# Optimization experiments

Measured on AMD Instinct MI355X. Metric: run time of the kernel, lower is better.

The kernel has to match this reference:

```python
import jax, jax.numpy as jnp
import numpy as np

NUM_BINS = 50


def _power_spectrum(x):
    # fft2 over last two dims, |.|^2, fftshift — matches torch.fft.fft2/fftshift
    freq = jnp.fft.fft2(x, axes=(-2, -1))
    power = jnp.abs(freq) ** 2
    return jnp.fft.fftshift(power, axes=(-2, -1))


def _radial_bin_ids(H, W, num_bins):
    # Static precompute of the bin index for every pixel (replaces the
    # triple-nested mask loop with a single segment reduction).
    cy, cx = H // 2, W // 2
    y = jnp.arange(H, dtype=jnp.float32) - cy
    x = jnp.arange(W, dtype=jnp.float32) - cx
    radius = jnp.sqrt(y[:, None] ** 2 + x[None, :] ** 2)  # [H, W]
    max_radius = min(H, W) // 2
    bin_edges = jnp.linspace(0.0, float(max_radius), num_bins + 1)
    # bin i covers [edges[i], edges[i+1]); radius >= max_radius -> overflow bin
    ids = jnp.clip(jnp.searchsorted(bin_edges, radius.ravel(), side='right') - 1, 0, num_bins)
    return ids  # [H*W], values in [0, num_bins] (num_bins = dropped overflow)


def _radial_profile(power, num_bins=NUM_BINS):
    B, C, H, W = power.shape
    ids = _radial_bin_ids(H, W, num_bins)
    pflat = power.reshape(B, C, H * W)
    seg_sum = jax.vmap(jax.vmap(lambda p: jax.ops.segment_sum(p, ids, num_segments=num_bins + 1)))(pflat)
    counts = jax.ops.segment_sum(jnp.ones((H * W,), power.dtype), ids, num_segments=num_bins + 1)
    profile = jnp.where(counts > 0, seg_sum / jnp.maximum(counts, 1.0), 0.0)
    return profile[..., :num_bins]  # [B, C, num_bins]


def setup_inputs() -> dict:
    key = jax.random.key(0)
    k1, k2 = jax.random.split(key)
    x = jax.random.normal(k1, (16, 3, 512, 512), dtype=jnp.float32)
    reference = jax.random.normal(k2, (16, 3, 512, 512), dtype=jnp.float32)
    return {"x": x, "reference": reference}


def reference(x, reference):
    power_x = _power_spectrum(x)
    profile_x = _radial_profile(power_x)
    power_ref = _power_spectrum(reference)
    profile_ref = _radial_profile(power_ref)
    B = profile_x.shape[0]
    logits_x = profile_x.reshape(B, -1)
    logits_ref = profile_ref.reshape(B, -1)
    # F.kl_div(log_p, q).sum(1) == sum q * (log q - log p)
    log_p = jax.nn.log_softmax(logits_x, axis=1)
    log_q = jax.nn.log_softmax(logits_ref, axis=1)
    q = jnp.exp(log_q)
    divergence = jnp.sum(q * (log_q - log_p), axis=1)  # [B]
    return divergence
```

## Files before the change

### kernel.cpp

```cpp
#include <hip/hip_runtime.h>


#define NIMG 96
#define NB 50
#define NCOL 257
#define PHYS(k) ((k) ^ (((k) >> 3) & 7))

typedef unsigned int uint32;
typedef unsigned short ushort16;

__device__ __forceinline__ float2 cadd(float2 a, float2 b){ return make_float2(a.x+b.x, a.y+b.y); }
__device__ __forceinline__ float2 csub(float2 a, float2 b){ return make_float2(a.x-b.x, a.y-b.y); }
__device__ __forceinline__ float2 cmul(float2 a, float2 b){
  return make_float2(fmaf(a.x, b.x, -(a.y*b.y)), fmaf(a.x, b.y, a.y*b.x));
}
__device__ __forceinline__ float2 mul_mi(float2 a){ return make_float2(a.y, -a.x); }

__device__ __forceinline__ uint32 bfpack(float re, float im) {
  uint32 ur = __float_as_uint(re); ur += 0x7FFFu + ((ur >> 16) & 1u);
  uint32 ui = __float_as_uint(im); ui += 0x7FFFu + ((ui >> 16) & 1u);
  return (ur & 0xFFFF0000u) | (ui >> 16);
}
__device__ __forceinline__ float2 bfunpack(uint32 u) {
  return make_float2(__uint_as_float(u & 0xFFFF0000u), __uint_as_float(u << 16));
}

struct C8 { float2 m0, m1, m2, m3, m4, m5, m6, m7; };

__device__ __forceinline__ C8 fft8(C8 v) {
  const float C = 0.70710678118654752f;
  float2 t0=cadd(v.m0,v.m4), t1=csub(v.m0,v.m4);
  float2 t2=cadd(v.m2,v.m6), t3m=mul_mi(csub(v.m2,v.m6));
  float2 E0=cadd(t0,t2), E1=cadd(t1,t3m), E2=csub(t0,t2), E3=csub(t1,t3m);
  float2 s0=cadd(v.m1,v.m5), s1=csub(v.m1,v.m5);
  float2 s2=cadd(v.m3,v.m7), s3m=mul_mi(csub(v.m3,v.m7));
  float2 O0=cadd(s0,s2), O1=cadd(s1,s3m), O2=csub(s0,s2), O3=csub(s1,s3m);
  O1 = make_float2(C*(O1.x+O1.y), C*(O1.y-O1.x));
  O2 = mul_mi(O2);
  O3 = make_float2(C*(O3.y-O3.x), -C*(O3.x+O3.y));
  C8 r;
  r.m0=cadd(E0,O0); r.m4=csub(E0,O0);
  r.m1=cadd(E1,O1); r.m5=csub(E1,O1);
  r.m2=cadd(E2,O2); r.m6=csub(E2,O2);
  r.m3=cadd(E3,O3); r.m7=csub(E3,O3);
  return r;
}

#define TWAP1(X, W) do { float2 t_ = (W);                               \
  X.m1=cmul(X.m1,t_); t_=cmul(t_,(W));                                  \
  X.m2=cmul(X.m2,t_); t_=cmul(t_,(W));                                  \
  X.m3=cmul(X.m3,t_); t_=cmul(t_,(W));                                  \
  X.m4=cmul(X.m4,t_); t_=cmul(t_,(W));                                  \
  X.m5=cmul(X.m5,t_); t_=cmul(t_,(W));                                  \
  X.m6=cmul(X.m6,t_); t_=cmul(t_,(W));                                  \
  X.m7=cmul(X.m7,t_); } while(0)

#define FFT512_1(X, Z, W1, W2, HI, LO) do {                                   \
  X = fft8(X);                                                                \
  TWAP1(X, W1);                                                               \
  Z[      8*((HI)^0)+(LO)] = X.m0;                                            \
  Z[ 64 + 8*((HI)^1)+(LO)] = X.m1;                                            \
  Z[128 + 8*((HI)^2)+(LO)] = X.m2;                                            \
  Z[192 + 8*((HI)^3)+(LO)] = X.m3;                                            \
  Z[256 + 8*((HI)^4)+(LO)] = X.m4;                                            \
  Z[320 + 8*((HI)^5)+(LO)] = X.m5;                                            \
  Z[384 + 8*((HI)^6)+(LO)] = X.m6;                                            \
  Z[448 + 8*((HI)^7)+(LO)] = X.m7;                                            \
  __builtin_amdgcn_wave_barrier();                                            \
  X.m0 = Z[64*(HI)+8*(0^(HI))+(LO)];                                          \
  X.m1 = Z[64*(HI)+8*(1^(HI))+(LO)];                                          \
  X.m2 = Z[64*(HI)+8*(2^(HI))+(LO)];                                          \
  X.m3 = Z[64*(HI)+8*(3^(HI))+(LO)];                                          \
  X.m4 = Z[64*(HI)+8*(4^(HI))+(LO)];                                          \
  X.m5 = Z[64*(HI)+8*(5^(HI))+(LO)];                                          \
  X.m6 = Z[64*(HI)+8*(6^(HI))+(LO)];                                          \
  X.m7 = Z[64*(HI)+8*(7^(HI))+(LO)];                                          \
  __builtin_amdgcn_wave_barrier();                                            \
  X = fft8(X);                                                                \
  TWAP1(X, W2);                                                               \
  Z[64*(HI)+8*(0^(HI))+((LO)^0)] = X.m0;                                      \
  Z[64*(HI)+8*(1^(HI))+((LO)^1)] = X.m1;                                      \
  Z[64*(HI)+8*(2^(HI))+((LO)^2)] = X.m2;                                      \
  Z[64*(HI)+8*(3^(HI))+((LO)^3)] = X.m3;                                      \
  Z[64*(HI)+8*(4^(HI))+((LO)^4)] = X.m4;                                      \
  Z[64*(HI)+8*(5^(HI))+((LO)^5)] = X.m5;                                      \
  Z[64*(HI)+8*(6^(HI))+((LO)^6)] = X.m6;                                      \
  Z[64*(HI)+8*(7^(HI))+((LO)^7)] = X.m7;                                      \
  __builtin_amdgcn_wave_barrier();                                            \
  X.m0 = Z[64*(HI)+8*((LO)^(HI))+(0^(LO))];                                   \
  X.m1 = Z[64*(HI)+8*((LO)^(HI))+(1^(LO))];                                   \
  X.m2 = Z[64*(HI)+8*((LO)^(HI))+(2^(LO))];                                   \
  X.m3 = Z[64*(HI)+8*((LO)^(HI))+(3^(LO))];                                   \
  X.m4 = Z[64*(HI)+8*((LO)^(HI))+(4^(LO))];                                   \
  X.m5 = Z[64*(HI)+8*((LO)^(HI))+(5^(LO))];                                   \
  X.m6 = Z[64*(HI)+8*((LO)^(HI))+(6^(LO))];                                   \
  X.m7 = Z[64*(HI)+8*((LO)^(HI))+(7^(LO))];                                   \
  __builtin_amdgcn_wave_barrier();                                            \
  X = fft8(X);                                                                \
} while(0)

#define TWIDDLE_W(W1, W2, lane)                                             \
  float2 W1, W2;                                                            \
  {                                                                         \
    float sv, cv;                                                           \
    __sincosf(-6.283185307179586f * (float)(lane) / 512.f, &sv, &cv);       \
    W1 = make_float2(cv, sv);                                               \
    __sincosf(-6.283185307179586f * (float)((lane) & 7) / 64.f, &sv, &cv);  \
    W2 = make_float2(cv, sv);                                               \
  }

__device__ __forceinline__ int binOf(int s, int cc) {
  return (int)(sqrtf((float)(s * s + cc * cc)) * 0.1953125f);
}
__device__ __forceinline__ int slo(int b, int cc) {
  if (b <= 0) return 0;
  float t = 26.2144f * (float)(b * b) - (float)(cc * cc);
  int s = (t <= 0.f) ? 0 : (int)ceilf(sqrtf(t));
  if (s > 257) s = 257;
  while (s > 0 && binOf(s - 1, cc) >= b) --s;
  while (s < 257 && binOf(s, cc) < b) ++s;
  return s;
}

__global__ __launch_bounds__(256) void build_slo_table(ushort16* __restrict__ tab)
{
  const int idx = blockIdx.x * 256 + threadIdx.x;
  if (idx >= NCOL * 51) return;
  const int c = idx / 51, b = idx - c * 51;
  tab[c * 52 + b] = (ushort16)slo(b, c);
}

__global__ __launch_bounds__(512, 8) void fft_rows_T(
    const float* __restrict__ xin, const float* __restrict__ rin,
    uint32* __restrict__ outT, int img0)
{
  __shared__ float2 s_z[8][516];
  const int tid = threadIdx.x, w = tid >> 6, lane = tid & 63;
  const int hi = lane >> 3, lo = lane & 7;
  const int imgL = blockIdx.x >> 5, blkin = blockIdx.x & 31;
  const int img = img0 + imgL;
  const float* base = (img < 48) ? (xin + (size_t)img * 262144)
                                 : (rin + (size_t)(img - 48) * 262144);
  const int rp = blkin * 8 + w;
  const float* src = base + (size_t)rp * 1024;

  TWIDDLE_W(w1, w2, lane)
  float2* z = s_z[w];
  uint32* outImg = outT + (size_t)imgL * ((size_t)NCOL * 512);

  C8 x;
  x.m0 = make_float2(src[      lane], src[512 +       lane]);
  x.m1 = make_float2(src[ 64 + lane], src[512 +  64 + lane]);
  x.m2 = make_float2(src[128 + lane], src[512 + 128 + lane]);
  x.m3 = make_float2(src[192 + lane], src[512 + 192 + lane]);
  x.m4 = make_float2(src[256 + lane], src[512 + 256 + lane]);
  x.m5 = make_float2(src[320 + lane], src[512 + 320 + lane]);
  x.m6 = make_float2(src[384 + lane], src[512 + 384 + lane]);
  x.m7 = make_float2(src[448 + lane], src[512 + 448 + lane]);

  FFT512_1(x, z, w1, w2, hi, lo);

  z[PHYS(hi + 8*lo +   0)] = x.m0;
  z[PHYS(hi + 8*lo +  64)] = x.m1;
  z[PHYS(hi + 8*lo + 128)] = x.m2;
  z[PHYS(hi + 8*lo + 192)] = x.m3;
  z[PHYS(hi + 8*lo + 256)] = x.m4;
  z[PHYS(hi + 8*lo + 320)] = x.m5;
  z[PHYS(hi + 8*lo + 384)] = x.m6;
  z[PHYS(hi + 8*lo + 448)] = x.m7;
  __builtin_amdgcn_wave_barrier();

#define SEPK(A, ST)                                                          \
  uint2 ST;                                                                  \
  {                                                                          \
    const int k  = 64 * (A) + lane;                                          \
    const int pk = (512 - k) & 511;                                          \
    float2 zk = z[PHYS(k)], zp = z[PHYS(pk)];                                \
    ST = make_uint2(bfpack(0.5f*(zk.x + zp.x), 0.5f*(zk.y - zp.y)),          \
                    bfpack(0.5f*(zk.y + zp.y), 0.5f*(zp.x - zk.x)));         \
  }
  SEPK(0, st0)
  SEPK(1, st1)
  SEPK(2, st2)
  SEPK(3, st3)
#undef SEPK
  float2 zn = z[256];
  __builtin_amdgcn_wave_barrier();

  uint2* zU = (uint2*)z;
  zU[       lane] = st0;
  zU[ 64 +  lane] = st1;
  zU[128 +  lane] = st2;
  zU[192 +  lane] = st3;
  __syncthreads();

  const int kk = tid >> 3, jj = tid & 7;
  const uint2* zUj = (const uint2*)(s_z[jj]);
  #pragma unroll
  for (int a = 0; a < 4; ++a) {
    uint2 v = zUj[64 * a + kk];
    *reinterpret_cast<uint2*>(outImg + ((size_t)(64 * a + kk) * 512
                                        + 16 * blkin + 2 * jj)) = v;
  }
  if (lane == 0) {
    *reinterpret_cast<uint2*>(outImg + ((size_t)256 * 512 + 2 * rp)) =
        make_uint2(bfpack(zn.x, 0.f), bfpack(zn.y, 0.f));
  }
}

__global__ __launch_bounds__(256, 8) void fft_cols_bin1(
    const uint32* __restrict__ inT, const ushort16* __restrict__ tab,
    float* __restrict__ profSum, int img0)
{
  __shared__ float2 s_z[4][512];
  __shared__ float s_bins[4][64];
  const int tid = threadIdx.x, w = tid >> 6, lane = tid & 63;
  const int hi = lane >> 3, lo = lane & 7;
  const int imgL = blockIdx.x / 65, blkin = blockIdx.x - imgL * 65;
  const int imgG = img0 + imgL;
  const int c  = blkin * 4 + w;
  const int cs = (c <= 256) ? c : 256;
  const float wf = (c > 256) ? 0.f : ((c == 0 || c == 256) ? 1.f : 2.f);

  TWIDDLE_W(w1, w2, lane)
  float2* z = s_z[w];
  const uint32* src = inT + ((size_t)(imgL * NCOL + cs)) * 512;
  C8 x;
  x.m0 = bfunpack(src[      lane]);
  x.m1 = bfunpack(src[ 64 + lane]);
  x.m2 = bfunpack(src[128 + lane]);
  x.m3 = bfunpack(src[192 + lane]);
  x.m4 = bfunpack(src[256 + lane]);
  x.m5 = bfunpack(src[320 + lane]);
  x.m6 = bfunpack(src[384 + lane]);
  x.m7 = bfunpack(src[448 + lane]);

  int ts0 = 0, ts1 = 0;
  if (lane < NB) {
    ts0 = tab[cs * 52 + lane];
    ts1 = tab[cs * 52 + lane + 1];
  }

  FFT512_1(x, z, w1, w2, hi, lo);

  float* zf = (float*)z;
  const int low6 = hi + 8 * lo;
  zf[low6      ] = x.m0.x*x.m0.x + x.m0.y*x.m0.y;
  zf[low6 +  64] = x.m1.x*x.m1.x + x.m1.y*x.m1.y;
  zf[low6 + 128] = x.m2.x*x.m2.x + x.m2.y*x.m2.y;
  zf[low6 + 192] = x.m3.x*x.m3.x + x.m3.y*x.m3.y;
  zf[low6 + 256] = x.m4.x*x.m4.x + x.m4.y*x.m4.y;
  zf[low6 + 320] = x.m5.x*x.m5.x + x.m5.y*x.m5.y;
  zf[low6 + 384] = x.m6.x*x.m6.x + x.m6.y*x.m6.y;
  zf[low6 + 448] = x.m7.x*x.m7.x + x.m7.y*x.m7.y;
  __builtin_amdgcn_wave_barrier();

  float4 a0 = *reinterpret_cast<float4*>(&zf[8 * lane]);
  float4 a1 = *reinterpret_cast<float4*>(&zf[8 * lane + 4]);

  a0.y += a0.x; a0.z += a0.y; a0.w += a0.z;
  a1.x += a0.w; a1.y += a1.x; a1.z += a1.y; a1.w += a1.z;
  float tot = a1.w;

  float s = tot;
  #pragma unroll
  for (int d = 1; d < 64; d <<= 1) {
    float t = __shfl_up(s, d);
    if (lane >= d) s += t;
  }
  float off = s - tot;
  a0.x += off; a0.y += off; a0.z += off; a0.w += off;
  a1.x += off; a1.y += off; a1.z += off; a1.w += off;

  *reinterpret_cast<float4*>(&zf[8 * lane])     = a0;
  *reinterpret_cast<float4*>(&zf[8 * lane + 4]) = a1;
  __builtin_amdgcn_wave_barrier();

  float acc = 0.f;
  if (lane < NB) {
    const int s0 = ts0, s1 = ts1;
    int hp = (s1 < 257 ? s1 : 257) - 1;
    float pos = ((hp >= 0) ? zf[hp] : 0.f) - ((s0 > 0) ? zf[s0 - 1] : 0.f);
    int sa = (s0 > 1) ? s0 : 1;
    int sb = (s1 - 1 < 255) ? (s1 - 1) : 255;
    float neg = (sb >= sa) ? (zf[512 - sa] - zf[511 - sb]) : 0.f;
    acc = wf * (pos + neg);
  }
  s_bins[w][lane] = acc;
  __syncthreads();
  if (tid < NB) {
    float ss = s_bins[0][tid] + s_bins[1][tid] + s_bins[2][tid] + s_bins[3][tid];
    atomicAdd(&profSum[(size_t)imgG * NB + tid], ss);
  }
}

__global__ __launch_bounds__(256) void compute_counts(float* __restrict__ cnt)
{
  const int t = threadIdx.x;
  __shared__ float lb[NB];
  if (t < NB) lb[t] = 0.f;
  __syncthreads();
  const int base = blockIdx.x * 2048;
  #pragma unroll
  for (int k = 0; k < 8; ++k) {
    const int idx = base + k * 256 + t;
    const int y  = idx >> 9;
    const int xx = idx & 511;
    const int sy = (y < 256) ? y : y - 512;
    const int sx = (xx < 256) ? xx : xx - 512;
    float r = sqrtf((float)(sy * sy + sx * sx));
    int bb = (int)(r * 0.1953125f);
    if (bb < NB) atomicAdd(&lb[bb], 1.f);
  }
  __syncthreads();
  if (t < NB) atomicAdd(&cnt[t], lb[t]);
}

__global__ __launch_bounds__(256) void finalize_kl(
    const float* __restrict__ profSum, const float* __restrict__ cntg,
    float* __restrict__ out)
{
  const int b = blockIdx.x;
  const int t = threadIdx.x;
  __shared__ float red[256];

  float lxv = -3.0e38f, lrv = -3.0e38f;
  if (t < 150) {
    const int cc  = t / NB;
    const int bin = t - cc * NB;
    const float c = cntg[bin];
    lxv = profSum[(size_t)(b * 3 + cc) * NB + bin] / c;
    lrv = profSum[(size_t)(48 + b * 3 + cc) * NB + bin] / c;
  }
  auto rmax = [&](float v) {
    red[t] = v; __syncthreads();
    for (int s2 = 128; s2 >= 1; s2 >>= 1) {
      if (t < s2) red[t] = fmaxf(red[t], red[t + s2]);
      __syncthreads();
    }
    float rr = red[0]; __syncthreads();
    return rr;
  };
  auto rsum = [&](float v) {
    red[t] = v; __syncthreads();
    for (int s2 = 128; s2 >= 1; s2 >>= 1) {
      if (t < s2) red[t] = red[t] + red[t + s2];
      __syncthreads();
    }
    float rr = red[0]; __syncthreads();
    return rr;
  };
  const float mx  = rmax(lxv);
  const float mr  = rmax(lrv);
  const float sx  = rsum((t < 150) ? expf(lxv - mx) : 0.f);
  const float sr  = rsum((t < 150) ? expf(lrv - mr) : 0.f);
  const float lsx = logf(sx);
  const float lsr = logf(sr);
  float term = 0.f;
  if (t < 150) {
    const float logp = lxv - mx - lsx;
    const float logq = lrv - mr - lsr;
    const float q    = expf(logq);
    term = q * (logq - logp);
  }
  const float div = rsum(term);
  if (t == 0) out[b] = div;
}

extern "C" void kernel_launch(void* const* d_in, const int* in_sizes, int n_in,
                              void* d_out, int out_size, void* d_ws, size_t ws_size,
                              hipStream_t stream)
{
  const float* x = (const float*)d_in[0];
  const float* r = (const float*)d_in[1];
  float* out     = (float*)d_out;

  float* profSum = (float*)d_ws;
  float* cnt     = (float*)((char*)d_ws + 19200);
  ushort16* tab  = (ushort16*)((char*)d_ws + 19456);
  const size_t IM_OFS = 46592;
  uint32* interT = (uint32*)((char*)d_ws + IM_OFS);

  const size_t perImg = (size_t)NCOL * 512 * sizeof(uint32);
  size_t avail = (ws_size > IM_OFS) ? (ws_size - IM_OFS) : 0;
  int ic = (int)(avail / perImg);
  if (ic > NIMG) ic = NIMG;
  if (ic < 1) ic = 1;

  hipMemsetAsync(d_ws, 0, 19456, stream);
  hipLaunchKernelGGL(build_slo_table, dim3(52), dim3(256), 0, stream, tab);
  hipLaunchKernelGGL(compute_counts, dim3(128), dim3(256), 0, stream, cnt);

  for (int img0 = 0; img0 < NIMG; img0 += ic) {
    const int n = (NIMG - img0 < ic) ? (NIMG - img0) : ic;
    hipLaunchKernelGGL(fft_rows_T, dim3(n * 32), dim3(512), 0, stream,
                       x, r, interT, img0);
    hipLaunchKernelGGL(fft_cols_bin1, dim3(n * 65), dim3(256), 0, stream,
                       interT, tab, profSum, img0);
  }
  hipLaunchKernelGGL(finalize_kl, dim3(16), dim3(256), 0, stream,
                     profSum, cnt, out);
}
```

Before: 69.22 us.

## Process two row-pairs per wave in row FFT to widen transposed stores

Result: slower. 214.3 us (+209.6%).

```diff
diff --git a/kernel.cpp b/kernel.cpp
--- a/kernel.cpp
+++ b/kernel.cpp
@@ -137,38 +137,38 @@
   __shared__ float2 s_z[8][516];
   const int tid = threadIdx.x, w = tid >> 6, lane = tid & 63;
   const int hi = lane >> 3, lo = lane & 7;
-  const int imgL = blockIdx.x >> 5, blkin = blockIdx.x & 31;
+  const int imgL = blockIdx.x >> 4, blkin = blockIdx.x & 15;
   const int img = img0 + imgL;
   const float* base = (img < 48) ? (xin + (size_t)img * 262144)
                                  : (rin + (size_t)(img - 48) * 262144);
-  const int rp = blkin * 8 + w;
-  const float* src = base + (size_t)rp * 1024;
+  const int rpA = blkin * 16 + w;
+  const int rpB = rpA + 8;
+  const float* srcA = base + (size_t)rpA * 1024;
+  const float* srcB = base + (size_t)rpB * 1024;
 
   TWIDDLE_W(w1, w2, lane)
   float2* z = s_z[w];
   uint32* outImg = outT + (size_t)imgL * ((size_t)NCOL * 512);
 
-  C8 x;
-  x.m0 = make_float2(src[      lane], src[512 +       lane]);
-  x.m1 = make_float2(src[ 64 + lane], src[512 +  64 + lane]);
-  x.m2 = make_float2(src[128 + lane], src[512 + 128 + lane]);
-  x.m3 = make_float2(src[192 + lane], src[512 + 192 + lane]);
-  x.m4 = make_float2(src[256 + lane], src[512 + 256 + lane]);
-  x.m5 = make_float2(src[320 + lane], src[512 + 320 + lane]);
-  x.m6 = make_float2(src[384 + lane], src[512 + 384 + lane]);
-  x.m7 = make_float2(src[448 + lane], src[512 + 448 + lane]);
-
-  FFT512_1(x, z, w1, w2, hi, lo);
-
-  z[PHYS(hi + 8*lo +   0)] = x.m0;
-  z[PHYS(hi + 8*lo +  64)] = x.m1;
-  z[PHYS(hi + 8*lo + 128)] = x.m2;
-  z[PHYS(hi + 8*lo + 192)] = x.m3;
-  z[PHYS(hi + 8*lo + 256)] = x.m4;
-  z[PHYS(hi + 8*lo + 320)] = x.m5;
-  z[PHYS(hi + 8*lo + 384)] = x.m6;
-  z[PHYS(hi + 8*lo + 448)] = x.m7;
-  __builtin_amdgcn_wave_barrier();
+#define LOADP(X, SRC)                                                        \
+  X.m0 = make_float2(SRC[      lane], SRC[512 +       lane]);                \
+  X.m1 = make_float2(SRC[ 64 + lane], SRC[512 +  64 + lane]);                \
+  X.m2 = make_float2(SRC[128 + lane], SRC[512 + 128 + lane]);                \
+  X.m3 = make_float2(SRC[192 + lane], SRC[512 + 192 + lane]);                \
+  X.m4 = make_float2(SRC[256 + lane], SRC[512 + 256 + lane]);                \
+  X.m5 = make_float2(SRC[320 + lane], SRC[512 + 320 + lane]);                \
+  X.m6 = make_float2(SRC[384 + lane], SRC[512 + 384 + lane]);                \
+  X.m7 = make_float2(SRC[448 + lane], SRC[512 + 448 + lane]);
+
+#define NATSTORE(X)                                                          \
+  z[PHYS(hi + 8*lo +   0)] = X.m0;                                           \
+  z[PHYS(hi + 8*lo +  64)] = X.m1;                                           \
+  z[PHYS(hi + 8*lo + 128)] = X.m2;                                           \
+  z[PHYS(hi + 8*lo + 192)] = X.m3;                                           \
+  z[PHYS(hi + 8*lo + 256)] = X.m4;                                           \
+  z[PHYS(hi + 8*lo + 320)] = X.m5;                                           \
+  z[PHYS(hi + 8*lo + 384)] = X.m6;                                           \
+  z[PHYS(hi + 8*lo + 448)] = X.m7;
 
 #define SEPK(A, ST)                                                          \
   uint2 ST;                                                                  \
@@ -179,32 +179,54 @@
     ST = make_uint2(bfpack(0.5f*(zk.x + zp.x), 0.5f*(zk.y - zp.y)),          \
                     bfpack(0.5f*(zk.y + zp.y), 0.5f*(zp.x - zk.x)));         \
   }
-  SEPK(0, st0)
-  SEPK(1, st1)
-  SEPK(2, st2)
-  SEPK(3, st3)
+
+  C8 x;
+  LOADP(x, srcA)
+  FFT512_1(x, z, w1, w2, hi, lo);
+  NATSTORE(x)
+  __builtin_amdgcn_wave_barrier();
+  SEPK(0, stA0) SEPK(1, stA1) SEPK(2, stA2) SEPK(3, stA3)
+  float2 znA = z[256];
+  __builtin_amdgcn_wave_barrier();
+
+  LOADP(x, srcB)
+  FFT512_1(x, z, w1, w2, hi, lo);
+  NATSTORE(x)
+  __builtin_amdgcn_wave_barrier();
+  SEPK(0, stB0) SEPK(1, stB1) SEPK(2, stB2) SEPK(3, stB3)
+  float2 znB = z[256];
+#undef LOADP
+#undef NATSTORE
 #undef SEPK
-  float2 zn = z[256];
-  __builtin_amdgcn_wave_barrier();
-
-  uint2* zU = (uint2*)z;
-  zU[       lane] = st0;
-  zU[ 64 +  lane] = st1;
-  zU[128 +  lane] = st2;
-  zU[192 +  lane] = st3;
   __syncthreads();
 
-  const int kk = tid >> 3, jj = tid & 7;
-  const uint2* zUj = (const uint2*)(s_z[jj]);
+  uint2* st = (uint2*)s_z;
+  st[0*1024 + lane*16 + ((w     + lane) & 15)] = stA0;
+  st[1*1024 + lane*16 + ((w     + lane) & 15)] = stA1;
+  st[2*1024 + lane*16 + ((w     + lane) & 15)] = stA2;
+  st[3*1024 + lane*16 + ((w     + lane) & 15)] = stA3;
+  st[0*1024 + lane*16 + ((w + 8 + lane) & 15)] = stB0;
+  st[1*1024 + lane*16 + ((w + 8 + lane) & 15)] = stB1;
+  st[2*1024 + lane*16 + ((w + 8 + lane) & 15)] = stB2;
+  st[3*1024 + lane*16 + ((w + 8 + lane) & 15)] = stB3;
+  __syncthreads();
+
+  const int kk0 = tid >> 4, p = tid & 15;
   #pragma unroll
   for (int a = 0; a < 4; ++a) {
-    uint2 v = zUj[64 * a + kk];
-    *reinterpret_cast<uint2*>(outImg + ((size_t)(64 * a + kk) * 512
-                                        + 16 * blkin + 2 * jj)) = v;
+    #pragma unroll
+    for (int h = 0; h < 2; ++h) {
+      const int kk = kk0 + 32 * h;
+      uint2 v = st[a*1024 + kk*16 + ((p + kk) & 15)];
+      *reinterpret_cast<uint2*>(outImg + ((size_t)(64*a + kk) * 512
+                                          + 32*blkin + 2*p)) = v;
+    }
   }
   if (lane == 0) {
-    *reinterpret_cast<uint2*>(outImg + ((size_t)256 * 512 + 2 * rp)) =
-        make_uint2(bfpack(zn.x, 0.f), bfpack(zn.y, 0.f));
+    *reinterpret_cast<uint2*>(outImg + ((size_t)256 * 512 + 2 * rpA)) =
+        make_uint2(bfpack(znA.x, 0.f), bfpack(znA.y, 0.f));
+    *reinterpret_cast<uint2*>(outImg + ((size_t)256 * 512 + 2 * rpB)) =
+        make_uint2(bfpack(znB.x, 0.f), bfpack(znB.y, 0.f));
   }
 }
 
@@ -393,7 +415,7 @@
 
   for (int img0 = 0; img0 < NIMG; img0 += ic) {
     const int n = (NIMG - img0 < ic) ? (NIMG - img0) : ic;
-    hipLaunchKernelGGL(fft_rows_T, dim3(n * 32), dim3(512), 0, stream,
+    hipLaunchKernelGGL(fft_rows_T, dim3(n * 16), dim3(512), 0, stream,
                        x, r, interT, img0);
     hipLaunchKernelGGL(fft_cols_bin1, dim3(n * 65), dim3(256), 0, stream,
                        interT, tab, profSum, img0);
```
